# Kernel tuning notes

Hardware: AMD Instinct MI355X
Metric: run time of the kernel (lower is better)

Reference implementation:

```python
import jax, jax.numpy as jnp
import numpy as np

D_MODEL = 2048
D_HID = 4096
N_EXPERTS = 8
TOP_K = 2
B, S = 2, 2048


def setup_inputs() -> dict:
    key = jax.random.key(0)
    ks = jax.random.split(key, 4)
    x = jax.random.normal(ks[0], (B, S, D_MODEL), dtype=jnp.float32)
    router_w = jax.random.normal(ks[1], (D_MODEL, N_EXPERTS), dtype=jnp.float32) * (D_MODEL ** -0.5)
    w1 = jax.random.normal(ks[2], (N_EXPERTS, D_MODEL, D_HID), dtype=jnp.float32) * (D_MODEL ** -0.5)
    b1 = jnp.zeros((N_EXPERTS, D_HID), dtype=jnp.float32)
    w2 = jax.random.normal(ks[3], (N_EXPERTS, D_HID, D_MODEL), dtype=jnp.float32) * (D_HID ** -0.5)
    b2 = jnp.zeros((N_EXPERTS, D_MODEL), dtype=jnp.float32)
    return {"x": x, "router_w": router_w, "w1": w1, "b1": b1, "w2": w2, "b2": b2}


def reference(x, router_w, w1, b1, w2, b2):
    # x: [B, S, D] -> tokens [T, D]
    Bc, Sc, D = x.shape
    xt = x.reshape(-1, D)                      # [T, D]
    T = xt.shape[0]
    E = w1.shape[0]

    # --- TopKRouter: linear gate -> softmax -> top-k, renormalized weights ---
    logits = xt @ router_w                     # [T, E]
    probs = jax.nn.softmax(logits, axis=-1)    # [T, E]
    weights, indices = jax.lax.top_k(probs, TOP_K)  # [T, K]
    weights = weights / jnp.sum(weights, axis=-1, keepdims=True)

    # Combine weights per (token, expert): sum over k-slots of weight * 1[idx==e]
    combine = jnp.zeros((T, E), dtype=xt.dtype).at[
        jnp.arange(T)[:, None], indices
    ].add(weights)                             # [T, E]

    # --- Expert FFNs: Linear -> GELU (exact, torch default) -> Linear ---
    out = jnp.zeros_like(xt)
    for e in range(E):  # small fixed loop over experts
        h = jax.nn.gelu(xt @ w1[e] + b1[e], approximate=False)  # [T, H]
        y = h @ w2[e] + b2[e]                                   # [T, D]
        out = out + combine[:, e:e + 1] * y

    return out.reshape(Bc, Sc, D)
```

## Files before the change

### kernel.cpp

```cpp
#include <hip/hip_runtime.h>

typedef unsigned short u16;
typedef unsigned int u32;
typedef short bf16x8 __attribute__((ext_vector_type(8)));
typedef float f32x4 __attribute__((ext_vector_type(4)));

#define T_TOK 4096
#define DM 2048
#define DH 4096
#define NE 8
#define MAXSLOT 9216
#define MAXTILE 72

#define OFF_META   128
#define OFF_TILEE  192
#define OFF_TOPE   512
#define OFF_TOPW   33280
#define OFF_SLOTT  66048
#define OFF_UNION  102912
#define OFF_XBF    139776
#define OFF_W1T    16916992ULL
#define OFF_W2T    151134720ULL
#define OFF_Y      285352448ULL
#define OFF_H3     323101184ULL
#define NEED_Y     324149760ULL

__device__ __forceinline__ u16 f2bf(float f) {
  union { float f; u32 u; } v; v.f = f;
  u32 r = v.u + 0x7fffu + ((v.u >> 16) & 1u);
  return (u16)(r >> 16);
}

__device__ __forceinline__ float bf2f(u16 h) {
  union { u32 u; float f; } v; v.u = ((u32)h) << 16; return v.f;
}

__device__ __forceinline__ float f4c(const float4& v, int c) {
  return c == 0 ? v.x : c == 1 ? v.y : c == 2 ? v.z : v.w;
}

__device__ __forceinline__ void gl_lds16(const u16* g, u16* l) {
  typedef __attribute__((address_space(1))) const u32 gu32;
  typedef __attribute__((address_space(3))) u32 lu32;
  __builtin_amdgcn_global_load_lds((gu32*)(const void*)g, (lu32*)(void*)l, 16, 0, 0);
}

__device__ __forceinline__ float gelu_f(float v) {
  float x = v * 0.70710678118654752f;
  float ax = fabsf(x);
  float t = 1.0f / fmaf(0.3275911f, ax, 1.0f);
  float p = t * fmaf(t, fmaf(t, fmaf(t, fmaf(t, 1.061405429f, -1.453152027f),
                                     1.421413741f), -0.284496736f), 0.254829592f);
  float er = 1.0f - p * __expf(-x * x);
  er = copysignf(er, x);
  return 0.5f * v * (1.0f + er);
}

__global__ __launch_bounds__(256) void prep_kernel(
    const float* __restrict__ x, const float* __restrict__ rw,
    const float* __restrict__ w1, const float* __restrict__ w2,
    int* __restrict__ counts, int* __restrict__ top_e, float* __restrict__ top_w,
    u16* __restrict__ xbf, u16* __restrict__ w1t, u16* __restrict__ w2t)
{
  __shared__ u16 T_s[4][64][64];
  int bid = blockIdx.x;
  if (bid < 8192) {
    const float* W; u16* Wt; int K, N, k0, n0;
    if (bid < 4096) {
      int e = bid >> 9, r = bid & 511;
      W = w1 + (size_t)e * DM * DH; Wt = w1t + (size_t)e * DM * DH;
      K = DM; N = DH; k0 = (r >> 4) * 64; n0 = (r & 15) * 256;
    } else {
      int b2 = bid - 4096;
      int e = b2 >> 9, r = b2 & 511;
      W = w2 + (size_t)e * DM * DH; Wt = w2t + (size_t)e * DM * DH;
      K = DH; N = DM; k0 = (r >> 3) * 64; n0 = (r & 7) * 256;
    }
    int wv = threadIdx.x >> 6, l = threadIdx.x & 63;
    int nw = n0 + wv * 64;
    const float* src = W + (size_t)k0 * N + nw + l;
#pragma unroll
    for (int h = 0; h < 2; ++h) {
      float v[32];
#pragma unroll
      for (int i = 0; i < 32; ++i) v[i] = src[(size_t)(h * 32 + i) * N];
#pragma unroll
      for (int j = 0; j < 4; ++j) {
        uint4 pk;
        pk.x = f2bf(v[j * 8 + 0]) | ((u32)f2bf(v[j * 8 + 1]) << 16);
        pk.y = f2bf(v[j * 8 + 2]) | ((u32)f2bf(v[j * 8 + 3]) << 16);
        pk.z = f2bf(v[j * 8 + 4]) | ((u32)f2bf(v[j * 8 + 5]) << 16);
        pk.w = f2bf(v[j * 8 + 6]) | ((u32)f2bf(v[j * 8 + 7]) << 16);
        int slot = ((h * 4 + j) + l) & 7;
        *(uint4*)&T_s[wv][l][slot * 8] = pk;
      }
    }
    __syncthreads();
#pragma unroll
    for (int r2 = 0; r2 < 8; ++r2) {
      int row = r2 * 8 + (l >> 3);
      int slot = ((l & 7) + row) & 7;
      uint4 vv = *(const uint4*)&T_s[wv][row][slot * 8];
      *(uint4*)(Wt + (size_t)(nw + row) * K + k0 + (l & 7) * 8) = vv;
    }
  } else if (bid < 8192 + 1024) {
    int wv = threadIdx.x >> 6;
    int lane = threadIdx.x & 63;
    int t = (bid - 8192) * 4 + wv;
    const float4* xr = (const float4*)(x + (size_t)t * DM);
    const float4* rw4 = (const float4*)rw;
    float acc[NE];
#pragma unroll
    for (int e = 0; e < NE; ++e) acc[e] = 0.f;
    for (int i = 0; i < 8; ++i) {
      int d4 = i * 64 + lane;
      float4 xv = xr[d4];
#pragma unroll
      for (int j = 0; j < 4; ++j) {
        int d = 4 * d4 + j;
        float4 r0 = rw4[d * 2];
        float4 r1 = rw4[d * 2 + 1];
        float xs = f4c(xv, j);
        acc[0] += xs * r0.x; acc[1] += xs * r0.y; acc[2] += xs * r0.z; acc[3] += xs * r0.w;
        acc[4] += xs * r1.x; acc[5] += xs * r1.y; acc[6] += xs * r1.z; acc[7] += xs * r1.w;
      }
    }
#pragma unroll
    for (int off = 32; off > 0; off >>= 1)
#pragma unroll
      for (int e = 0; e < NE; ++e) acc[e] += __shfl_xor(acc[e], off, 64);
    if (lane == 0) {
      int e0 = 0; float l0 = acc[0];
#pragma unroll
      for (int e = 1; e < NE; ++e) if (acc[e] > l0) { l0 = acc[e]; e0 = e; }
      int e1 = -1; float l1 = -3.0e38f;
#pragma unroll
      for (int e = 0; e < NE; ++e) if (e != e0 && acc[e] > l1) { l1 = acc[e]; e1 = e; }
      float w0 = 1.f / (1.f + expf(l1 - l0));
      float w1v = 1.f - w0;
      top_e[t * 2 + 0] = e0; top_e[t * 2 + 1] = e1;
      top_w[t * 2 + 0] = w0; top_w[t * 2 + 1] = w1v;
      atomicAdd(&counts[e0], 1);
      atomicAdd(&counts[e1], 1);
    }
  } else {
    size_t i = ((size_t)(bid - 9216) * 256 + threadIdx.x) * 8;
    float4 a = *(const float4*)(x + i);
    float4 b = *(const float4*)(x + i + 4);
    union { uint4 u; u16 s[8]; } o;
    o.s[0] = f2bf(a.x); o.s[1] = f2bf(a.y); o.s[2] = f2bf(a.z); o.s[3] = f2bf(a.w);
    o.s[4] = f2bf(b.x); o.s[5] = f2bf(b.y); o.s[6] = f2bf(b.z); o.s[7] = f2bf(b.w);
    *(uint4*)(xbf + i) = o.u;
  }
}

__global__ void scan_kernel(int* __restrict__ wsI)
{
  int* counts = wsI;
  int* curs   = wsI + 8;
  int* offs   = wsI + 16;
  int* meta   = wsI + (OFF_META / 4);
  int* tile_e = wsI + (OFF_TILEE / 4);
  int* slot_token = wsI + (OFF_SLOTT / 4);
  float* slot_wt = (float*)(wsI + (OFF_UNION / 4));
  __shared__ int s_off[9];
  if (threadIdx.x == 0) {
    int o = 0;
    for (int e = 0; e < NE; ++e) {
      offs[e] = o; curs[e] = o; s_off[e] = o;
      o += (counts[e] + 127) & ~127;
    }
    offs[8] = o; s_off[8] = o;
    meta[0] = o >> 7;
  }
  __syncthreads();
  int nt = s_off[8] >> 7;
  for (int i = threadIdx.x; i < MAXTILE; i += blockDim.x) {
    int e = -1;
    if (i < nt) {
      for (int j = 0; j < NE; ++j)
        if (i * 128 >= s_off[j] && i * 128 < s_off[j + 1]) e = j;
    }
    tile_e[i] = e;
  }
  for (int i = threadIdx.x; i < MAXSLOT; i += blockDim.x) {
    slot_token[i] = -1;
    slot_wt[i] = 0.f;
  }
}

__global__ void scatter_kernel(const int* __restrict__ top_e, const float* __restrict__ top_w,
                               int* __restrict__ curs, int* __restrict__ slot_token,
                               int* __restrict__ tok_slots, float* __restrict__ slot_wt,
                               int useY)
{
  int t = blockIdx.x * blockDim.x + threadIdx.x;
  if (t >= T_TOK) return;
#pragma unroll
  for (int k = 0; k < 2; ++k) {
    int e = top_e[t * 2 + k];
    int pos = atomicAdd(&curs[e], 1);
    slot_token[pos] = t;
    if (useY) tok_slots[t * 2 + k] = pos;
    else      slot_wt[pos] = top_w[t * 2 + k];
  }
}


#define GATEN(n) asm volatile("s_waitcnt vmcnt(" #n ")" ::: "memory")
#define NOGATE ((void)0)
#define NOSTG  ((void)0)
#define NORD   ((void)0)

#define SA_(PA, KO) do { \
  gl_lds16(aptr0 + (KO), &PA[wid * 16][0]);        \
  gl_lds16(aptr1 + (KO), &PA[64 + wid * 16][0]); } while (0)
#define SB1_(PB, KO) gl_lds16(bptr0 + (KO), &PB[wid * 16][0])
#define SB2_(PB, KO) do { \
  gl_lds16(bptr1 + (KO), &PB[64 + wid * 16][0]);   \
  gl_lds16(bptr2 + (KO), &PB[128 + wid * 16][0]);  \
  gl_lds16(bptr3 + (KO), &PB[192 + wid * 16][0]); } while (0)

#define RDAF(S, P, H)                                                   \
  _Pragma("unroll")                                                     \
  for (int i_ = 0; i_ < 4; ++i_)                                        \
    S[i_] = *(const bf16x8*)&P[(H) * 64 + i_ * 16 + lrow][sp8]
#define RDBF(S, P)                                                      \
  _Pragma("unroll")                                                     \
  for (int n_ = 0; n_ < 4; ++n_)                                        \
    S[n_] = *(const bf16x8*)&P[wn + n_ * 16 + lrow][sp8]

#define PH(AFC, BFRC, MHc, STG, GATE, ...) do {                         \
  STG;                                                                  \
  GATE;                                                                 \
  __builtin_amdgcn_s_barrier();                                         \
  asm volatile("s_waitcnt lgkmcnt(0)" ::: "memory");                    \
  __builtin_amdgcn_sched_barrier(0);                                    \
  __builtin_amdgcn_s_setprio(1);                                        \
  _Pragma("unroll")                                                     \
  for (int nf = 0; nf < 4; ++nf)                                        \
    _Pragma("unroll")                                                   \
    for (int i = 0; i < 4; ++i)                                         \
      acc[nf][(MHc) * 4 + i] = __builtin_amdgcn_mfma_f32_16x16x32_bf16( \
          BFRC[nf], AFC[i], acc[nf][(MHc) * 4 + i], 0, 0, 0);           \
  __builtin_amdgcn_s_setprio(0);                                        \
  __VA_ARGS__;                                                          \
  __builtin_amdgcn_s_barrier();                                         \
  __builtin_amdgcn_sched_barrier(0);                                    \
} while (0)

template<int MODE, int EPI>
__global__ __launch_bounds__(256, 2) void gemm_tb(
    const u16* __restrict__ Wt, const float* __restrict__ bias,
    const u16* __restrict__ Abase,
    u16* __restrict__ Hout, u16* __restrict__ Ybuf, float* __restrict__ Out,
    const int* __restrict__ slot_token, const float* __restrict__ slot_wt,
    const int* __restrict__ tile_e, const int* __restrict__ meta,
    int tile0, int mtc)
{
  constexpr int KD = (MODE == 0) ? DM : DH;
  constexpr int ND = (MODE == 0) ? DH : DM;
  constexpr int NT = ND / 256;
  constexpr int NK = KD / 32;

  __shared__ u16 A_s[3][128][32];
  __shared__ u16 B_s[3][256][32];

  int nwg = gridDim.x;
  int flat = blockIdx.x;
  int q8 = nwg >> 3, rr = nwg & 7;
  int xcd = flat & 7, i0 = flat >> 3;
  int wg = (xcd < rr ? xcd * (q8 + 1) : rr * (q8 + 1) + (xcd - rr) * q8) + i0;
  int mloc = wg / NT;
  int ntile = wg % NT;
  int mt = tile0 + mloc;
  if (mt >= meta[0]) return;
  int e = tile_e[mt];
  int n0 = ntile * 256;

  const int tid = threadIdx.x;
  const int lane = tid & 63;
  const int wid = tid >> 6;
  const int lrow = lane & 15;
  const int g = lane >> 4;
  const int sp8 = (g ^ ((lrow >> 1) & 3)) << 3;
  const int wn = wid << 6;

  const int srow = tid >> 2;
  const int swz = ((tid & 3) ^ ((tid >> 3) & 3)) << 3;

  const u16 *aptr0, *aptr1;
  if (MODE == 0) {
    int t0 = slot_token[mt * 128 + srow];       if (t0 < 0) t0 = 0;
    int t1 = slot_token[mt * 128 + 64 + srow];  if (t1 < 0) t1 = 0;
    aptr0 = Abase + (size_t)t0 * KD + swz;
    aptr1 = Abase + (size_t)t1 * KD + swz;
  } else {
    aptr0 = Abase + (size_t)(mloc * 128 + srow) * KD + swz;
    aptr1 = Abase + (size_t)(mloc * 128 + 64 + srow) * KD + swz;
  }
  const u16* bptr0 = Wt + ((size_t)e * ND + n0 + srow) * KD + swz;
  const u16* bptr1 = bptr0 + (size_t)64 * KD;
  const u16* bptr2 = bptr0 + (size_t)128 * KD;
  const u16* bptr3 = bptr0 + (size_t)192 * KD;

  f32x4 acc[4][8] = {};
  bf16x8 afX[4], afY[4], bfrA[4], bfrB[4];

  u16 (*pA0)[32] = A_s[0]; u16 (*pA1)[32] = A_s[1]; u16 (*pA2)[32] = A_s[2];
  u16 (*pB0)[32] = B_s[0]; u16 (*pB1)[32] = B_s[1]; u16 (*pB2)[32] = B_s[2];

  SA_(pA0, 0); SB1_(pB0, 0); SB2_(pB0, 0);
  SA_(pA1, 32); SB1_(pB1, 32); SB2_(pB1, 32);
  GATEN(6);
  __builtin_amdgcn_s_barrier();
  __builtin_amdgcn_sched_barrier(0);
  RDAF(afX, pA0, 0);
  RDBF(bfrA, pB0);

  for (int t = 0; t < NK - 3; t += 2) {
    int ko2 = (t + 2) * 32, ko3 = (t + 3) * 32;
    PH(afX, bfrA, 0, SA_(pA2, ko2); SB1_(pB2, ko2), NOGATE,
       RDAF(afY, pA0, 1));
    PH(afY, bfrA, 1, SB2_(pB2, ko2), GATEN(6),
       RDAF(afX, pA1, 0); RDBF(bfrB, pB1));
    PH(afX, bfrB, 0, SA_(pA0, ko3); SB1_(pB0, ko3), NOGATE,
       RDAF(afY, pA1, 1));
    PH(afY, bfrB, 1, SB2_(pB0, ko3), GATEN(6),
       RDAF(afX, pA2, 0); RDBF(bfrA, pB2));
    u16 (*tA)[32] = pA0; pA0 = pA2; pA2 = pA1; pA1 = tA;
    u16 (*tB)[32] = pB0; pB0 = pB2; pB2 = pB1; pB1 = tB;
  }
  {
    PH(afX, bfrA, 0, NOSTG, NOGATE, RDAF(afY, pA0, 1));
    PH(afY, bfrA, 1, NOSTG, GATEN(0), RDAF(afX, pA1, 0); RDBF(bfrB, pB1));
    PH(afX, bfrB, 0, NOSTG, NOGATE, RDAF(afY, pA1, 1));
    PH(afY, bfrB, 1, NOSTG, NOGATE, NORD);
  }

  const int rb = g << 2;
  float4 bias4[4];
#pragma unroll
  for (int nf = 0; nf < 4; ++nf)
    bias4[nf] = *(const float4*)&bias[e * ND + n0 + wn + nf * 16 + rb];

  if constexpr (MODE == 0) {
#pragma unroll
    for (int mf = 0; mf < 8; ++mf) {
      u16* hp = Hout + (size_t)(mloc * 128 + mf * 16 + lrow) * DH + n0 + wn + rb;
#pragma unroll
      for (int nf = 0; nf < 4; ++nf) {
        float v0 = gelu_f(acc[nf][mf][0] + bias4[nf].x);
        float v1 = gelu_f(acc[nf][mf][1] + bias4[nf].y);
        float v2 = gelu_f(acc[nf][mf][2] + bias4[nf].z);
        float v3 = gelu_f(acc[nf][mf][3] + bias4[nf].w);
        uint2 pk;
        pk.x = f2bf(v0) | ((u32)f2bf(v1) << 16);
        pk.y = f2bf(v2) | ((u32)f2bf(v3) << 16);
        *(uint2*)(hp + nf * 16) = pk;
      }
    }
  } else if constexpr (EPI == 0) {
#pragma unroll
    for (int mf = 0; mf < 8; ++mf) {
      u16* yp = Ybuf + (size_t)(mt * 128 + mf * 16 + lrow) * DM + n0 + wn + rb;
#pragma unroll
      for (int nf = 0; nf < 4; ++nf) {
        float v0 = acc[nf][mf][0] + bias4[nf].x;
        float v1 = acc[nf][mf][1] + bias4[nf].y;
        float v2 = acc[nf][mf][2] + bias4[nf].z;
        float v3 = acc[nf][mf][3] + bias4[nf].w;
        uint2 pk;
        pk.x = f2bf(v0) | ((u32)f2bf(v1) << 16);
        pk.y = f2bf(v2) | ((u32)f2bf(v3) << 16);
        *(uint2*)(yp + nf * 16) = pk;
      }
    }
  } else {
#pragma unroll
    for (int mf = 0; mf < 8; ++mf) {
      int gs = mt * 128 + mf * 16 + lrow;
      int tok = slot_token[gs];
      if (tok < 0) continue;
      float wt = slot_wt[gs];
      float* op = Out + (size_t)tok * DM + n0 + wn + rb;
#pragma unroll
      for (int nf = 0; nf < 4; ++nf) {
        atomicAdd(op + nf * 16 + 0, wt * (acc[nf][mf][0] + bias4[nf].x));
        atomicAdd(op + nf * 16 + 1, wt * (acc[nf][mf][1] + bias4[nf].y));
        atomicAdd(op + nf * 16 + 2, wt * (acc[nf][mf][2] + bias4[nf].z));
        atomicAdd(op + nf * 16 + 3, wt * (acc[nf][mf][3] + bias4[nf].w));
      }
    }
  }
}

__global__ __launch_bounds__(256) void combine_kernel(
    const u16* __restrict__ y, const int* __restrict__ tok_slots,
    const float* __restrict__ top_w, float* __restrict__ out)
{
  int t = blockIdx.x;
  int d = threadIdx.x * 8;
  int s0 = tok_slots[t * 2], s1 = tok_slots[t * 2 + 1];
  float w0 = top_w[t * 2], w1 = top_w[t * 2 + 1];
  union { uint4 u; u16 s[8]; } a, b;
  a.u = *(const uint4*)(y + (size_t)s0 * DM + d);
  b.u = *(const uint4*)(y + (size_t)s1 * DM + d);
  float o[8];
#pragma unroll
  for (int j = 0; j < 8; ++j) o[j] = w0 * bf2f(a.s[j]) + w1 * bf2f(b.s[j]);
  float* op = out + (size_t)t * DM + d;
  *(float4*)op = make_float4(o[0], o[1], o[2], o[3]);
  *(float4*)(op + 4) = make_float4(o[4], o[5], o[6], o[7]);
}

extern "C" void kernel_launch(void* const* d_in, const int* in_sizes, int n_in,
                              void* d_out, int out_size, void* d_ws, size_t ws_size,
                              hipStream_t stream) {
  const float* x  = (const float*)d_in[0];
  const float* rw = (const float*)d_in[1];
  const float* w1 = (const float*)d_in[2];
  const float* b1 = (const float*)d_in[3];
  const float* w2 = (const float*)d_in[4];
  const float* b2 = (const float*)d_in[5];
  float* out = (float*)d_out;
  char* ws = (char*)d_ws;

  int* counts = (int*)ws;
  int* curs   = (int*)(ws + 32);
  int* meta   = (int*)(ws + OFF_META);
  int* tile_e = (int*)(ws + OFF_TILEE);
  int* top_e  = (int*)(ws + OFF_TOPE);
  float* top_w = (float*)(ws + OFF_TOPW);
  int* slot_token = (int*)(ws + OFF_SLOTT);
  int* tok_slots  = (int*)(ws + OFF_UNION);
  float* slot_wt  = (float*)(ws + OFF_UNION);
  u16* xbf = (u16*)(ws + OFF_XBF);
  u16* w1t = (u16*)(ws + OFF_W1T);
  u16* w2t = (u16*)(ws + OFF_W2T);

  const int useY = (ws_size >= NEED_Y) ? 1 : 0;
  u16* ybuf = (u16*)(ws + OFF_Y);
  u16* hbuf = (u16*)(ws + (useY ? OFF_H3 : OFF_Y));

  hipMemsetAsync(ws, 0, 512, stream);
  if (!useY) hipMemsetAsync(d_out, 0, (size_t)out_size * sizeof(float), stream);

  prep_kernel<<<13312, 256, 0, stream>>>(x, rw, w1, w2, counts, top_e, top_w,
                                         xbf, w1t, w2t);
  scan_kernel<<<1, 256, 0, stream>>>((int*)ws);
  scatter_kernel<<<T_TOK / 256, 256, 0, stream>>>(top_e, top_w, curs, slot_token,
                                                  tok_slots, slot_wt, useY);

  size_t hoff = useY ? OFF_H3 : OFF_Y;
  size_t avail = ws_size > hoff ? ws_size - hoff : (size_t)DH * 256;
  long ch_slots = (long)(avail / (DH * 2));
  ch_slots = (ch_slots / 128) * 128;
  if (ch_slots > MAXSLOT) ch_slots = MAXSLOT;
  if (ch_slots < 128) ch_slots = 128;
  int mtc = (int)(ch_slots / 128);
  int nchunks = (MAXTILE + mtc - 1) / mtc;

  for (int c = 0; c < nchunks; ++c) {
    int tile0 = c * mtc;
    gemm_tb<0, 0><<<dim3(mtc * (DH / 256)), 256, 0, stream>>>(
        w1t, b1, xbf, hbuf, nullptr, nullptr, slot_token, slot_wt, tile_e, meta, tile0, mtc);
    if (useY) {
      gemm_tb<1, 0><<<dim3(mtc * (DM / 256)), 256, 0, stream>>>(
          w2t, b2, hbuf, nullptr, ybuf, nullptr, slot_token, slot_wt, tile_e, meta, tile0, mtc);
    } else {
      gemm_tb<1, 1><<<dim3(mtc * (DM / 256)), 256, 0, stream>>>(
          w2t, b2, hbuf, nullptr, nullptr, out, slot_token, slot_wt, tile_e, meta, tile0, mtc);
    }
  }
  if (useY)
    combine_kernel<<<T_TOK, 256, 0, stream>>>(ybuf, tok_slots, top_w, out);
}
```

Measured before the change: 707.1 us.

## Fuse bf16 conversion of x into router blocks and simplify GEMM k-loop pipeline

The router blocks in the prep kernel now also write the bf16 copy of x while reading it, so the separate conversion blocks are removed and x is read once instead of twice. The GEMM main loop changes from four half-phases per two k-steps, with split A/B fragment registers, to one full phase per k-step. Each phase issues all stores for the next stage, waits, then runs 32 MFMAs with all 8 A fragments and 4 B fragments. This halves the barrier count and simplifies scheduling. It also reduces interleaving of global loads with compute and may change register pressure.

```diff
diff --git a/kernel.cpp b/kernel.cpp
--- a/kernel.cpp
+++ b/kernel.cpp
@@ -103,7 +103,7 @@
       uint4 vv = *(const uint4*)&T_s[wv][row][slot * 8];
       *(uint4*)(Wt + (size_t)(nw + row) * K + k0 + (l & 7) * 8) = vv;
     }
-  } else if (bid < 8192 + 1024) {
+  } else {
     int wv = threadIdx.x >> 6;
     int lane = threadIdx.x & 63;
     int t = (bid - 8192) * 4 + wv;
@@ -115,6 +115,10 @@
     for (int i = 0; i < 8; ++i) {
       int d4 = i * 64 + lane;
       float4 xv = xr[d4];
+      uint2 pk;
+      pk.x = f2bf(xv.x) | ((u32)f2bf(xv.y) << 16);
+      pk.y = f2bf(xv.z) | ((u32)f2bf(xv.w) << 16);
+      *(uint2*)(xbf + (size_t)t * DM + d4 * 4) = pk;
 #pragma unroll
       for (int j = 0; j < 4; ++j) {
         int d = 4 * d4 + j;
@@ -143,14 +147,6 @@
       atomicAdd(&counts[e0], 1);
       atomicAdd(&counts[e1], 1);
     }
-  } else {
-    size_t i = ((size_t)(bid - 9216) * 256 + threadIdx.x) * 8;
-    float4 a = *(const float4*)(x + i);
-    float4 b = *(const float4*)(x + i + 4);
-    union { uint4 u; u16 s[8]; } o;
-    o.s[0] = f2bf(a.x); o.s[1] = f2bf(a.y); o.s[2] = f2bf(a.z); o.s[3] = f2bf(a.w);
-    o.s[4] = f2bf(b.x); o.s[5] = f2bf(b.y); o.s[6] = f2bf(b.z); o.s[7] = f2bf(b.w);
-    *(uint4*)(xbf + i) = o.u;
   }
 }
 
@@ -221,16 +217,16 @@
   gl_lds16(bptr2 + (KO), &PB[128 + wid * 16][0]);  \
   gl_lds16(bptr3 + (KO), &PB[192 + wid * 16][0]); } while (0)
 
-#define RDAF(S, P, H)                                                   \
+#define RDAF8(P)                                                        \
   _Pragma("unroll")                                                     \
-  for (int i_ = 0; i_ < 4; ++i_)                                        \
-    S[i_] = *(const bf16x8*)&P[(H) * 64 + i_ * 16 + lrow][sp8]
-#define RDBF(S, P)                                                      \
+  for (int i_ = 0; i_ < 8; ++i_)                                        \
+    af[i_] = *(const bf16x8*)&P[i_ * 16 + lrow][sp8]
+#define RDBF(P)                                                         \
   _Pragma("unroll")                                                     \
   for (int n_ = 0; n_ < 4; ++n_)                                        \
-    S[n_] = *(const bf16x8*)&P[wn + n_ * 16 + lrow][sp8]
-
-#define PH(AFC, BFRC, MHc, STG, GATE, ...) do {                         \
+    bfr[n_] = *(const bf16x8*)&P[wn + n_ * 16 + lrow][sp8]
+
+#define PHF(STG, GATE, RD) do {                                         \
   STG;                                                                  \
   GATE;                                                                 \
   __builtin_amdgcn_s_barrier();                                         \
@@ -240,11 +236,11 @@
   _Pragma("unroll")                                                     \
   for (int nf = 0; nf < 4; ++nf)                                        \
     _Pragma("unroll")                                                   \
-    for (int i = 0; i < 4; ++i)                                         \
-      acc[nf][(MHc) * 4 + i] = __builtin_amdgcn_mfma_f32_16x16x32_bf16( \
-          BFRC[nf], AFC[i], acc[nf][(MHc) * 4 + i], 0, 0, 0);           \
+    for (int mf = 0; mf < 8; ++mf)                                      \
+      acc[nf][mf] = __builtin_amdgcn_mfma_f32_16x16x32_bf16(            \
+          bfr[nf], af[mf], acc[nf][mf], 0, 0, 0);                       \
   __builtin_amdgcn_s_setprio(0);                                        \
-  __VA_ARGS__;                                                          \
+  RD;                                                                   \
   __builtin_amdgcn_s_barrier();                                         \
   __builtin_amdgcn_sched_barrier(0);                                    \
 } while (0)
@@ -305,7 +301,7 @@
   const u16* bptr3 = bptr0 + (size_t)192 * KD;
 
   f32x4 acc[4][8] = {};
-  bf16x8 afX[4], afY[4], bfrA[4], bfrB[4];
+  bf16x8 af[8], bfr[4];
 
   u16 (*pA0)[32] = A_s[0]; u16 (*pA1)[32] = A_s[1]; u16 (*pA2)[32] = A_s[2];
   u16 (*pB0)[32] = B_s[0]; u16 (*pB1)[32] = B_s[1]; u16 (*pB2)[32] = B_s[2];
@@ -315,28 +311,18 @@
   GATEN(6);
   __builtin_amdgcn_s_barrier();
   __builtin_amdgcn_sched_barrier(0);
-  RDAF(afX, pA0, 0);
-  RDBF(bfrA, pB0);
-
-  for (int t = 0; t < NK - 3; t += 2) {
-    int ko2 = (t + 2) * 32, ko3 = (t + 3) * 32;
-    PH(afX, bfrA, 0, SA_(pA2, ko2); SB1_(pB2, ko2), NOGATE,
-       RDAF(afY, pA0, 1));
-    PH(afY, bfrA, 1, SB2_(pB2, ko2), GATEN(6),
-       RDAF(afX, pA1, 0); RDBF(bfrB, pB1));
-    PH(afX, bfrB, 0, SA_(pA0, ko3); SB1_(pB0, ko3), NOGATE,
-       RDAF(afY, pA1, 1));
-    PH(afY, bfrB, 1, SB2_(pB0, ko3), GATEN(6),
-       RDAF(afX, pA2, 0); RDBF(bfrA, pB2));
-    u16 (*tA)[32] = pA0; pA0 = pA2; pA2 = pA1; pA1 = tA;
-    u16 (*tB)[32] = pB0; pB0 = pB2; pB2 = pB1; pB1 = tB;
-  }
-  {
-    PH(afX, bfrA, 0, NOSTG, NOGATE, RDAF(afY, pA0, 1));
-    PH(afY, bfrA, 1, NOSTG, GATEN(0), RDAF(afX, pA1, 0); RDBF(bfrB, pB1));
-    PH(afX, bfrB, 0, NOSTG, NOGATE, RDAF(afY, pA1, 1));
-    PH(afY, bfrB, 1, NOSTG, NOGATE, NORD);
-  }
+  RDAF8(pA0);
+  RDBF(pB0);
+
+  for (int t = 0; t < NK - 2; ++t) {
+    int ko = (t + 2) * 32;
+    PHF(SA_(pA2, ko); SB1_(pB2, ko); SB2_(pB2, ko), GATEN(6),
+        RDAF8(pA1); RDBF(pB1));
+    u16 (*tA)[32] = pA0; pA0 = pA1; pA1 = pA2; pA2 = tA;
+    u16 (*tB)[32] = pB0; pB0 = pB1; pB1 = pB2; pB2 = tB;
+  }
+  PHF(NOSTG, GATEN(0), RDAF8(pA1); RDBF(pB1));
+  PHF(NOSTG, NOGATE, NORD);
 
   const int rb = g << 2;
   float4 bias4[4];
@@ -446,8 +432,8 @@
   hipMemsetAsync(ws, 0, 512, stream);
   if (!useY) hipMemsetAsync(d_out, 0, (size_t)out_size * sizeof(float), stream);
 
-  prep_kernel<<<13312, 256, 0, stream>>>(x, rw, w1, w2, counts, top_e, top_w,
-                                         xbf, w1t, w2t);
+  prep_kernel<<<9216, 256, 0, stream>>>(x, rw, w1, w2, counts, top_e, top_w,
+                                        xbf, w1t, w2t);
   scan_kernel<<<1, 256, 0, stream>>>((int*)ws);
   scatter_kernel<<<T_TOK / 256, 256, 0, stream>>>(top_e, top_w, curs, slot_token,
                                                   tok_slots, slot_wt, useY);
```

New measurement: 700.6 us. Within noise of the previous version (-0.9%).
